# Optimization experiments

Measured on AMD Instinct MI355X. Metric: run time of the kernel, lower is better.

The kernel has to match this reference:

```python
import jax, jax.numpy as jnp
import numpy as np

B, N, D, H = 4, 8192, 1024, 8
HD = D // H  # 128
EPS = 1e-5


def setup_inputs() -> dict:
    key = jax.random.key(0)
    k1, k2, k3 = jax.random.split(key, 3)
    x = jax.random.normal(k1, (B, N, D), dtype=jnp.float32)
    mask = jax.random.randint(k2, (B, 1, N), 0, 2).astype(jnp.bool_)
    # nn.Linear(dim, 3*dim, bias=False): weight [3D, D]; store as [D, 3D] for x @ w
    w_qkv = jax.random.normal(k3, (D, 3 * D), dtype=jnp.float32) / np.sqrt(D)
    gamma = jnp.ones((D,), dtype=jnp.float32)
    beta = jnp.zeros((D,), dtype=jnp.float32)
    return {"x": x, "mask": mask, "w_qkv": w_qkv, "gamma": gamma, "beta": beta}


def _layernorm(x, gamma, beta):
    mu = jnp.mean(x, axis=-1, keepdims=True)
    var = jnp.mean(jnp.square(x - mu), axis=-1, keepdims=True)
    return (x - mu) * jax.lax.rsqrt(var + EPS) * gamma + beta


def reference(x, mask, w_qkv, gamma, beta):
    xn = _layernorm(x, gamma, beta)                       # [B,N,D]
    qkv = xn @ w_qkv                                      # [B,N,3D]
    q, k, v = jnp.split(qkv, 3, axis=-1)
    # 'b n (h d) -> b h n d'
    def to_heads(t):
        return t.reshape(B, N, H, HD).transpose(0, 2, 1, 3)
    q, k, v = to_heads(q), to_heads(k), to_heads(v)       # [B,H,N,HD]
    q = jax.nn.sigmoid(q)
    k = jnp.tanh(k)
    k = jnp.where(mask[..., None], 0.0, k)                # masked_fill -> 0
    kv = jnp.einsum('bhnd,bhne->bhde', k, v)              # k^T @ v, [B,H,HD,HD]
    out = jnp.einsum('bhnd,bhde->bhne', q, kv)            # [B,H,N,HD]
    out = out.transpose(0, 2, 1, 3).reshape(B, N, D)      # 'b h n d -> b n (h d)'
    return out  # output_layer='None' -> Identity
```

## Files before the change

### kernel.cpp

```cpp
#include <hip/hip_runtime.h>

#define EPS 1e-5f
#define B_ 4
#define N_ 8192
#define D_ 1024
#define H_ 8
#define HD_ 128
#define M_TOT 32768
#define NQKV 3072

typedef __bf16 bf16x8 __attribute__((ext_vector_type(8)));
typedef float f32x4 __attribute__((ext_vector_type(4)));

__device__ __forceinline__ float bf2f(unsigned short u) {
    unsigned int v = ((unsigned int)u) << 16;
    return __uint_as_float(v);
}
__device__ __forceinline__ unsigned short f2bf(float f) {
    unsigned int u = __float_as_uint(f);
    u += 0x7fffu + ((u >> 16) & 1u);
    return (unsigned short)(u >> 16);
}

__device__ __forceinline__ float fast_sigmoid(float v) {
    return __builtin_amdgcn_rcpf(1.0f + __expf(-v));
}
__device__ __forceinline__ float fast_tanh(float v) {
    return 1.0f - 2.0f * __builtin_amdgcn_rcpf(1.0f + __expf(2.0f * v));
}

__device__ __forceinline__ void gl_lds16(const void* g, void* l) {
    __builtin_amdgcn_global_load_lds(
        (const __attribute__((address_space(1))) unsigned int*)g,
        (__attribute__((address_space(3))) unsigned int*)l, 16, 0, 0);
}

__global__ __launch_bounds__(256) void ln_kernel(const float* __restrict__ x,
                                                 const float* __restrict__ gamma,
                                                 const float* __restrict__ beta,
                                                 unsigned short* __restrict__ xn) {
    const int row = blockIdx.x * 4 + (threadIdx.x >> 6);
    const int t = threadIdx.x & 63;
    const float* xr = x + (size_t)row * D_;
    float4 xv[4];
    #pragma unroll
    for (int i = 0; i < 4; i++) xv[i] = ((const float4*)xr)[i * 64 + t];
    float s = 0.0f, s2 = 0.0f;
    #pragma unroll
    for (int i = 0; i < 4; i++) {
        s  += xv[i].x + xv[i].y + xv[i].z + xv[i].w;
        s2 += xv[i].x * xv[i].x + xv[i].y * xv[i].y
            + xv[i].z * xv[i].z + xv[i].w * xv[i].w;
    }
    #pragma unroll
    for (int off = 32; off > 0; off >>= 1) {
        s  += __shfl_down(s, off);
        s2 += __shfl_down(s2, off);
    }
    s = __shfl(s, 0);
    s2 = __shfl(s2, 0);
    const float mu = s * (1.0f / D_);
    const float var = s2 * (1.0f / D_) - mu * mu;
    const float rs = rsqrtf(var + EPS);
    unsigned short* xo = xn + (size_t)row * D_;
    #pragma unroll
    for (int i = 0; i < 4; i++) {
        float4 g  = ((const float4*)gamma)[i * 64 + t];
        float4 bt = ((const float4*)beta)[i * 64 + t];
        ushort4 o;
        o.x = f2bf((xv[i].x - mu) * rs * g.x + bt.x);
        o.y = f2bf((xv[i].y - mu) * rs * g.y + bt.y);
        o.z = f2bf((xv[i].z - mu) * rs * g.z + bt.z);
        o.w = f2bf((xv[i].w - mu) * rs * g.w + bt.w);
        ((ushort4*)xo)[i * 64 + t] = o;
    }
}

__global__ __launch_bounds__(256) void wt_kernel(const float* __restrict__ w,
                                                 unsigned short* __restrict__ wT) {
    __shared__ float tile[64][65];
    const int n0 = blockIdx.x * 64;
    const int k0 = blockIdx.y * 64;
    const int t = threadIdx.x;
    const int tx = t & 63, ty = t >> 6;
    #pragma unroll
    for (int i = 0; i < 16; i++) {
        int r = i * 4 + ty;
        tile[r][tx] = w[(size_t)(k0 + r) * NQKV + n0 + tx];
    }
    __syncthreads();
    #pragma unroll
    for (int i = 0; i < 16; i++) {
        int r = i * 4 + ty;
        wT[(size_t)(n0 + r) * D_ + k0 + tx] = f2bf(tile[tx][r]);
    }
}

#define CT_STRIDE 136
__global__ __launch_bounds__(256, 3) void qkv_gemm(const unsigned short* __restrict__ xn,
                                                   const unsigned short* __restrict__ wT,
                                                   const int* __restrict__ mask,
                                                   unsigned short* __restrict__ qws,
                                                   unsigned short* __restrict__ kT,
                                                   unsigned short* __restrict__ vT) {
    __shared__ unsigned short ShB[128 * CT_STRIDE];
    const int t = threadIdx.x;
    const int w = t >> 6, l = t & 63;
    const int quad = l >> 4, ln16 = l & 15;
    const int m0 = blockIdx.y * 128;
    const int n0 = blockIdx.x * 128;
    const int wm = (w >> 1) * 64, wn = (w & 1) * 64;

    f32x4 acc[4][4] = {};

    const unsigned short* aG = xn + (size_t)(m0 + w * 16 + (l >> 2)) * D_ + (l & 3) * 8;
    const unsigned short* bG = wT + (size_t)(n0 + w * 16 + (l >> 2)) * D_ + (l & 3) * 8;
    char* SB = (char*)ShB;

    for (int k0 = 0; k0 < 1024; k0 += 64) {
        #pragma unroll
        for (int s = 0; s < 2; s++) {
            gl_lds16(aG + k0 + s * 32,            SB + s * 8192 + w * 1024);
            gl_lds16(aG + 64 * D_ + k0 + s * 32,  SB + s * 8192 + 4096 + w * 1024);
            gl_lds16(bG + k0 + s * 32,            SB + 16384 + s * 8192 + w * 1024);
            gl_lds16(bG + 64 * D_ + k0 + s * 32,  SB + 16384 + s * 8192 + 4096 + w * 1024);
        }
        __syncthreads();
        #pragma unroll
        for (int s = 0; s < 2; s++) {
            const char* A0 = SB + s * 8192;
            const char* B0 = SB + 16384 + s * 8192;
            bf16x8 af[4], bfr[4];
            #pragma unroll
            for (int mi = 0; mi < 4; mi++)
                af[mi] = *(const bf16x8*)(A0 + (wm + mi * 16 + ln16) * 64 + quad * 16);
            #pragma unroll
            for (int ni = 0; ni < 4; ni++)
                bfr[ni] = *(const bf16x8*)(B0 + (wn + ni * 16 + ln16) * 64 + quad * 16);
            #pragma unroll
            for (int mi = 0; mi < 4; mi++)
                #pragma unroll
                for (int ni = 0; ni < 4; ni++)
                    acc[mi][ni] = __builtin_amdgcn_mfma_f32_16x16x32_bf16(af[mi], bfr[ni],
                                                                          acc[mi][ni], 0, 0, 0);
        }
        __syncthreads();
    }

    const int region = n0 >> 10;
    const int cbase = n0 & 1023;
    if (region == 0) {
        #pragma unroll
        for (int mi = 0; mi < 4; mi++) {
            #pragma unroll
            for (int r = 0; r < 4; r++) {
                int gm = m0 + wm + mi * 16 + quad * 4 + r;
                #pragma unroll
                for (int ni = 0; ni < 4; ni++) {
                    int cc = cbase + wn + ni * 16 + ln16;
                    qws[(size_t)gm * D_ + cc] = f2bf(fast_sigmoid(acc[mi][ni][r]));
                }
            }
        }
    } else {
        #pragma unroll
        for (int mi = 0; mi < 4; mi++) {
            int tok0 = wm + mi * 16 + quad * 4;
            int mk0 = 0, mk1 = 0, mk2 = 0, mk3 = 0;
            if (region == 1) {
                mk0 = mask[m0 + tok0];
                mk1 = mask[m0 + tok0 + 1];
                mk2 = mask[m0 + tok0 + 2];
                mk3 = mask[m0 + tok0 + 3];
            }
            #pragma unroll
            for (int ni = 0; ni < 4; ni++) {
                int fl = wn + ni * 16 + ln16;
                float v0 = acc[mi][ni][0], v1 = acc[mi][ni][1];
                float v2 = acc[mi][ni][2], v3 = acc[mi][ni][3];
                if (region == 1) {
                    v0 = mk0 ? 0.0f : fast_tanh(v0);
                    v1 = mk1 ? 0.0f : fast_tanh(v1);
                    v2 = mk2 ? 0.0f : fast_tanh(v2);
                    v3 = mk3 ? 0.0f : fast_tanh(v3);
                }
                ushort4 pk;
                pk.x = f2bf(v0); pk.y = f2bf(v1); pk.z = f2bf(v2); pk.w = f2bf(v3);
                *(ushort4*)&ShB[fl * CT_STRIDE + tok0] = pk;
            }
        }
        __syncthreads();
        unsigned short* dstT = (region == 1) ? kT : vT;
        const int h = cbase >> 7;
        const int b = m0 >> 13;
        const int ntok0 = m0 & 8191;
        #pragma unroll
        for (int p = 0; p < 8; p++) {
            int fl = p * 16 + (t >> 4);
            int tok = (t & 15) * 8;
            uint4 u = *(const uint4*)&ShB[fl * CT_STRIDE + tok];
            *(uint4*)(dstT + ((size_t)(b * 8 + h) * 128 + fl) * 8192 + ntok0 + tok) = u;
        }
    }
}

__global__ __launch_bounds__(256) void kv_mfma(const unsigned short* __restrict__ kT,
                                               const unsigned short* __restrict__ vT,
                                               float* __restrict__ kvp) {
    __shared__ __align__(16) char smem[32768];
    char* AsB = smem;
    char* BsB = smem + 16384;
    const int t = threadIdx.x;
    const int w = t >> 6, l = t & 63;
    const int quad = l >> 4, ln16 = l & 15;
    const int bh = blockIdx.y;
    const int kc0 = blockIdx.x * 256;
    const int wm = (w >> 1) * 64, wn = (w & 1) * 64;

    f32x4 acc[4][4] = {};

    const size_t base = (size_t)bh * 128 * 8192;
    const int gsw = (l & 7) ^ (l >> 3);
    const unsigned short* aG = kT + base + (size_t)(w * 8 + (l >> 3)) * 8192 + kc0 + gsw * 8;
    const unsigned short* bG = vT + base + (size_t)(w * 8 + (l >> 3)) * 8192 + kc0 + gsw * 8;
    const int r7 = ln16 & 7;
    const int kb0 = ((quad ^ r7) << 4);
    const int kb1 = (((4 | quad) ^ r7) << 4);

    for (int kk = 0; kk < 256; kk += 64) {
        #pragma unroll
        for (int c = 0; c < 4; c++) {
            gl_lds16(aG + (size_t)(c * 32) * 8192 + kk, AsB + c * 4096 + w * 1024);
            gl_lds16(bG + (size_t)(c * 32) * 8192 + kk, BsB + c * 4096 + w * 1024);
        }
        __syncthreads();
        bf16x8 af[4][2], bfr[4][2];
        #pragma unroll
        for (int mi = 0; mi < 4; mi++) {
            const char* rp = AsB + (wm + mi * 16 + ln16) * 128;
            af[mi][0] = *(const bf16x8*)(rp + kb0);
            af[mi][1] = *(const bf16x8*)(rp + kb1);
        }
        #pragma unroll
        for (int ni = 0; ni < 4; ni++) {
            const char* rp = BsB + (wn + ni * 16 + ln16) * 128;
            bfr[ni][0] = *(const bf16x8*)(rp + kb0);
            bfr[ni][1] = *(const bf16x8*)(rp + kb1);
        }
        #pragma unroll
        for (int mi = 0; mi < 4; mi++)
            #pragma unroll
            for (int ni = 0; ni < 4; ni++) {
                acc[mi][ni] = __builtin_amdgcn_mfma_f32_16x16x32_bf16(af[mi][0], bfr[ni][0],
                                                                      acc[mi][ni], 0, 0, 0);
                acc[mi][ni] = __builtin_amdgcn_mfma_f32_16x16x32_bf16(af[mi][1], bfr[ni][1],
                                                                      acc[mi][ni], 0, 0, 0);
            }
        __syncthreads();
    }

    float* dst = kvp + ((size_t)blockIdx.x * 32 + bh) * (HD_ * HD_);
    #pragma unroll
    for (int mi = 0; mi < 4; mi++) {
        #pragma unroll
        for (int r = 0; r < 4; r++) {
            int d = wm + mi * 16 + quad * 4 + r;
            #pragma unroll
            for (int ni = 0; ni < 4; ni++) {
                int e = wn + ni * 16 + ln16;
                dst[d * HD_ + e] = acc[mi][ni][r];
            }
        }
    }
}

__global__ __launch_bounds__(256) void kvcvt(const float* __restrict__ kvp,
                                             unsigned short* __restrict__ kvTb) {
    __shared__ float tile[32][132];
    const int bh = blockIdx.x;
    const int c = blockIdx.y;
    const int t = threadIdx.x;
    {
        int r = t >> 3, cc = (t & 7) * 16;
        f32x4 s[4] = {};
        for (int p = 0; p < 32; p++) {
            const float* src = kvp + ((size_t)p * 32 + bh) * (HD_ * HD_)
                               + (size_t)(c * 32 + r) * 128 + cc;
            #pragma unroll
            for (int q4 = 0; q4 < 4; q4++)
                s[q4] += *(const f32x4*)(src + q4 * 4);
        }
        #pragma unroll
        for (int q4 = 0; q4 < 4; q4++)
            *(f32x4*)&tile[r][cc + q4 * 4] = s[q4];
    }
    __syncthreads();
    {
        int e = t >> 1, dh = t & 1;
        ushort4 o[4];
        #pragma unroll
        for (int q4 = 0; q4 < 4; q4++) {
            o[q4].x = f2bf(tile[dh * 16 + q4 * 4 + 0][e]);
            o[q4].y = f2bf(tile[dh * 16 + q4 * 4 + 1][e]);
            o[q4].z = f2bf(tile[dh * 16 + q4 * 4 + 2][e]);
            o[q4].w = f2bf(tile[dh * 16 + q4 * 4 + 3][e]);
        }
        unsigned short* dst = kvTb + (size_t)bh * 16384 + e * 128 + c * 32 + dh * 16;
        #pragma unroll
        for (int q4 = 0; q4 < 4; q4++)
            ((ushort4*)dst)[q4] = o[q4];
    }
}

__global__ __launch_bounds__(256) void out_mfma(const unsigned short* __restrict__ qws,
                                                const unsigned short* __restrict__ kvTb,
                                                float* __restrict__ out) {
    __shared__ __align__(16) char smem[32768];
    char* AsB = smem;
    const int t = threadIdx.x;
    const int w = t >> 6, l = t & 63;
    const int quad = l >> 4, ln16 = l & 15;
    const int m0 = blockIdx.x * 128;
    const int h = blockIdx.y;
    const int b = m0 >> 13;
    const int bh = b * 8 + h;
    const int wm = (w >> 1) * 64, wn = (w & 1) * 64;

    const int gsw = (l & 15) ^ (w * 4 + (l >> 4));
    const unsigned short* aG = qws + (size_t)(m0 + w * 4 + (l >> 4)) * D_
                               + h * HD_ + gsw * 8;
    #pragma unroll
    for (int c = 0; c < 8; c++)
        gl_lds16(aG + (size_t)(c * 16) * D_, AsB + c * 4096 + w * 1024);

    const char* bB = (const char*)kvTb + (size_t)bh * 32768;

    __syncthreads();

    f32x4 acc[4][4] = {};
    #pragma unroll
    for (int ks = 0; ks < 4; ks++) {
        bf16x8 af[4], bfr[4];
        #pragma unroll
        for (int ni = 0; ni < 4; ni++)
            bfr[ni] = *(const bf16x8*)(bB + (wn + ni * 16 + ln16) * 256
                                       + ks * 64 + quad * 16);
        #pragma unroll
        for (int mi = 0; mi < 4; mi++)
            af[mi] = *(const bf16x8*)(AsB + (wm + mi * 16 + ln16) * 256
                                      + ((((ks * 4) + quad) ^ ln16) << 4));
        #pragma unroll
        for (int mi = 0; mi < 4; mi++)
            #pragma unroll
            for (int ni = 0; ni < 4; ni++)
                acc[mi][ni] = __builtin_amdgcn_mfma_f32_16x16x32_bf16(af[mi], bfr[ni],
                                                                      acc[mi][ni], 0, 0, 0);
    }

    #pragma unroll
    for (int mi = 0; mi < 4; mi++) {
        #pragma unroll
        for (int r = 0; r < 4; r++) {
            int gm = m0 + wm + mi * 16 + quad * 4 + r;
            #pragma unroll
            for (int ni = 0; ni < 4; ni++) {
                int e = wn + ni * 16 + ln16;
                out[(size_t)gm * D_ + h * HD_ + e] = acc[mi][ni][r];
            }
        }
    }
}

extern "C" void kernel_launch(void* const* d_in, const int* in_sizes, int n_in,
                              void* d_out, int out_size, void* d_ws, size_t ws_size,
                              hipStream_t stream) {
    const float* x     = (const float*)d_in[0];
    const int*   mask  = (const int*)d_in[1];
    const float* w     = (const float*)d_in[2];
    const float* gamma = (const float*)d_in[3];
    const float* beta  = (const float*)d_in[4];
    float* out = (float*)d_out;
    char* ws = (char*)d_ws;

    unsigned short* xn  = (unsigned short*)(ws + 0);
    unsigned short* wT  = (unsigned short*)(ws + 67108864ull);
    unsigned short* qws = (unsigned short*)(ws + 73400320ull);
    unsigned short* kT  = (unsigned short*)(ws + 140509184ull);
    unsigned short* vT  = (unsigned short*)(ws + 207618048ull);
    unsigned short* kvTb = (unsigned short*)(ws + 274726912ull);
    float* kvp = (float*)(ws + 0);

    hipLaunchKernelGGL(ln_kernel, dim3(M_TOT / 4), dim3(256), 0, stream, x, gamma, beta, xn);
    hipLaunchKernelGGL(wt_kernel, dim3(48, 16), dim3(256), 0, stream, w, wT);
    hipLaunchKernelGGL(qkv_gemm, dim3(NQKV / 128, M_TOT / 128), dim3(256), 0, stream,
                       xn, wT, mask, qws, kT, vT);
    hipLaunchKernelGGL(kv_mfma, dim3(32, 32), dim3(256), 0, stream, kT, vT, kvp);
    hipLaunchKernelGGL(kvcvt, dim3(32, 4), dim3(256), 0, stream, kvp, kvTb);
    hipLaunchKernelGGL(out_mfma, dim3(M_TOT / 128, 8), dim3(256), 0, stream,
                       qws, kvTb, out);
}
```

Baseline: 538.7 us.

## Load MFMA fragments directly from global memory in kv and out kernels

Drops the LDS staging, async global-to-LDS copies and barriers in kv_mfma and out_mfma, so each wave loads its bf16x8 MFMA fragments straight from global memory. kv_mfma also doubles its per-block token chunk from 256 to 512, which halves the grid and the number of partial kv tiles kvcvt has to reduce. Global loads become strided and less coalesced, and data reuse across waves now relies on the caches, with fewer blocks in flight for kv_mfma.

```diff
diff --git a/kernel.cpp b/kernel.cpp
--- a/kernel.cpp
+++ b/kernel.cpp
@@ -207,45 +207,33 @@
 __global__ __launch_bounds__(256) void kv_mfma(const unsigned short* __restrict__ kT,
                                                const unsigned short* __restrict__ vT,
                                                float* __restrict__ kvp) {
-    __shared__ __align__(16) char smem[32768];
-    char* AsB = smem;
-    char* BsB = smem + 16384;
     const int t = threadIdx.x;
     const int w = t >> 6, l = t & 63;
     const int quad = l >> 4, ln16 = l & 15;
     const int bh = blockIdx.y;
-    const int kc0 = blockIdx.x * 256;
+    const int kc0 = blockIdx.x * 512;
     const int wm = (w >> 1) * 64, wn = (w & 1) * 64;
 
     f32x4 acc[4][4] = {};
 
     const size_t base = (size_t)bh * 128 * 8192;
-    const int gsw = (l & 7) ^ (l >> 3);
-    const unsigned short* aG = kT + base + (size_t)(w * 8 + (l >> 3)) * 8192 + kc0 + gsw * 8;
-    const unsigned short* bG = vT + base + (size_t)(w * 8 + (l >> 3)) * 8192 + kc0 + gsw * 8;
-    const int r7 = ln16 & 7;
-    const int kb0 = ((quad ^ r7) << 4);
-    const int kb1 = (((4 | quad) ^ r7) << 4);
-
-    for (int kk = 0; kk < 256; kk += 64) {
-        #pragma unroll
-        for (int c = 0; c < 4; c++) {
-            gl_lds16(aG + (size_t)(c * 32) * 8192 + kk, AsB + c * 4096 + w * 1024);
-            gl_lds16(bG + (size_t)(c * 32) * 8192 + kk, BsB + c * 4096 + w * 1024);
-        }
-        __syncthreads();
+    const unsigned short* aBase = kT + base + kc0 + quad * 8;
+    const unsigned short* bBase = vT + base + kc0 + quad * 8;
+
+    #pragma unroll 2
+    for (int kk = 0; kk < 512; kk += 64) {
         bf16x8 af[4][2], bfr[4][2];
         #pragma unroll
         for (int mi = 0; mi < 4; mi++) {
-            const char* rp = AsB + (wm + mi * 16 + ln16) * 128;
-            af[mi][0] = *(const bf16x8*)(rp + kb0);
-            af[mi][1] = *(const bf16x8*)(rp + kb1);
+            const unsigned short* p = aBase + (size_t)(wm + mi * 16 + ln16) * 8192 + kk;
+            af[mi][0] = *(const bf16x8*)(p);
+            af[mi][1] = *(const bf16x8*)(p + 32);
         }
         #pragma unroll
         for (int ni = 0; ni < 4; ni++) {
-            const char* rp = BsB + (wn + ni * 16 + ln16) * 128;
-            bfr[ni][0] = *(const bf16x8*)(rp + kb0);
-            bfr[ni][1] = *(const bf16x8*)(rp + kb1);
+            const unsigned short* p = bBase + (size_t)(wn + ni * 16 + ln16) * 8192 + kk;
+            bfr[ni][0] = *(const bf16x8*)(p);
+            bfr[ni][1] = *(const bf16x8*)(p + 32);
         }
         #pragma unroll
         for (int mi = 0; mi < 4; mi++)
@@ -256,7 +244,6 @@
                 acc[mi][ni] = __builtin_amdgcn_mfma_f32_16x16x32_bf16(af[mi][1], bfr[ni][1],
                                                                       acc[mi][ni], 0, 0, 0);
             }
-        __syncthreads();
     }
 
     float* dst = kvp + ((size_t)blockIdx.x * 32 + bh) * (HD_ * HD_);
@@ -283,7 +270,7 @@
     {
         int r = t >> 3, cc = (t & 7) * 16;
         f32x4 s[4] = {};
-        for (int p = 0; p < 32; p++) {
+        for (int p = 0; p < 16; p++) {
             const float* src = kvp + ((size_t)p * 32 + bh) * (HD_ * HD_)
                                + (size_t)(c * 32 + r) * 128 + cc;
             #pragma unroll
@@ -315,8 +302,6 @@
 __global__ __launch_bounds__(256) void out_mfma(const unsigned short* __restrict__ qws,
                                                 const unsigned short* __restrict__ kvTb,
                                                 float* __restrict__ out) {
-    __shared__ __align__(16) char smem[32768];
-    char* AsB = smem;
     const int t = threadIdx.x;
     const int w = t >> 6, l = t & 63;
     const int quad = l >> 4, ln16 = l & 15;
@@ -326,29 +311,20 @@
     const int bh = b * 8 + h;
     const int wm = (w >> 1) * 64, wn = (w & 1) * 64;
 
-    const int gsw = (l & 15) ^ (w * 4 + (l >> 4));
-    const unsigned short* aG = qws + (size_t)(m0 + w * 4 + (l >> 4)) * D_
-                               + h * HD_ + gsw * 8;
-    #pragma unroll
-    for (int c = 0; c < 8; c++)
-        gl_lds16(aG + (size_t)(c * 16) * D_, AsB + c * 4096 + w * 1024);
-
-    const char* bB = (const char*)kvTb + (size_t)bh * 32768;
-
-    __syncthreads();
-
     f32x4 acc[4][4] = {};
+
+    const unsigned short* aBase = qws + (size_t)m0 * D_ + h * HD_ + quad * 8;
+    const unsigned short* bBase = kvTb + (size_t)bh * 16384 + quad * 8;
+
     #pragma unroll
     for (int ks = 0; ks < 4; ks++) {
         bf16x8 af[4], bfr[4];
         #pragma unroll
+        for (int mi = 0; mi < 4; mi++)
+            af[mi] = *(const bf16x8*)(aBase + (size_t)(wm + mi * 16 + ln16) * D_ + ks * 32);
+        #pragma unroll
         for (int ni = 0; ni < 4; ni++)
-            bfr[ni] = *(const bf16x8*)(bB + (wn + ni * 16 + ln16) * 256
-                                       + ks * 64 + quad * 16);
-        #pragma unroll
-        for (int mi = 0; mi < 4; mi++)
-            af[mi] = *(const bf16x8*)(AsB + (wm + mi * 16 + ln16) * 256
-                                      + ((((ks * 4) + quad) ^ ln16) << 4));
+            bfr[ni] = *(const bf16x8*)(bBase + (wn + ni * 16 + ln16) * 128 + ks * 32);
         #pragma unroll
         for (int mi = 0; mi < 4; mi++)
             #pragma unroll
@@ -394,7 +370,7 @@
     hipLaunchKernelGGL(wt_kernel, dim3(48, 16), dim3(256), 0, stream, w, wT);
     hipLaunchKernelGGL(qkv_gemm, dim3(NQKV / 128, M_TOT / 128), dim3(256), 0, stream,
                        xn, wT, mask, qws, kT, vT);
-    hipLaunchKernelGGL(kv_mfma, dim3(32, 32), dim3(256), 0, stream, kT, vT, kvp);
+    hipLaunchKernelGGL(kv_mfma, dim3(16, 32), dim3(256), 0, stream, kT, vT, kvp);
     hipLaunchKernelGGL(kvcvt, dim3(32, 4), dim3(256), 0, stream, kvp, kvTb);
     hipLaunchKernelGGL(out_mfma, dim3(M_TOT / 128, 8), dim3(256), 0, stream,
                        qws, kvTb, out);
```

After: 558.3 us. 3.6% more time.
